# Kernel optimization log

Hardware: AMD Instinct MI355X
Metric: run time of the kernel (lower is better)

Reference implementation:

```python
import jax, jax.numpy as jnp
import numpy as np

B, W, N, L = 64, 256, 128, 64


def setup_inputs() -> dict:
    key = jax.random.key(0)
    k1, k2, k3 = jax.random.split(key, 3)
    x = jax.random.normal(k1, (B, W, L), dtype=jnp.float32)
    shapelets = jax.random.normal(k2, (N, L), dtype=jnp.float32)
    cls_w = jax.random.normal(k3, (1, N), dtype=jnp.float32) * 0.1
    cls_b = jnp.zeros((1,), dtype=jnp.float32)
    return {"x": x, "shapelets": shapelets, "cls_w": cls_w, "cls_b": cls_b}


def reference(x, shapelets, cls_w, cls_b):
    # diffs: [B, W, N, L] broadcast subtract
    diffs = x[:, :, None, :] - shapelets[None, None, :, :]
    # L2 norm over shapelet-length axis -> [B, W, N]
    discrim = jnp.sqrt(jnp.sum(diffs * diffs, axis=3))
    # min over windows -> [B, N]
    min_discrim = jnp.min(discrim, axis=1)
    # tiny classifier: Linear(N, 1) + sigmoid -> [B, 1]
    logits = min_discrim @ cls_w.T + cls_b
    return jax.nn.sigmoid(logits)
```

## Files before the change

kernel.cpp:

```cpp
#include <hip/hip_runtime.h>
#include <cfloat>
#include <cmath>

constexpr int B = 64;
constexpr int W = 256;
constexpr int N = 128;
constexpr int L = 64;
constexpr int NC = 16;
constexpr int WPB = W / NC;

__global__ __launch_bounds__(256) void shapelet_min_kernel(
    const float* __restrict__ x, const float* __restrict__ shp,
    float* __restrict__ part) {
  __shared__ float xs[WPB * L];
  __shared__ float xnorm_s[WPB];

  const int b = blockIdx.x >> 4;
  const int c = blockIdx.x & 15;
  const int tid = threadIdx.x;
  const int n = tid >> 1;
  const int half = tid & 1;

  {
    const float4* xg =
        (const float4*)(x + ((size_t)b * W + (size_t)c * WPB) * L);
    float4 v = xg[tid];
    ((float4*)xs)[tid] = v;
    float p = v.x * v.x + v.y * v.y + v.z * v.z + v.w * v.w;
    p += __shfl_xor(p, 8, 16);
    p += __shfl_xor(p, 4, 16);
    p += __shfl_xor(p, 2, 16);
    p += __shfl_xor(p, 1, 16);
    if ((tid & 15) == 0) xnorm_s[tid >> 4] = p;
  }

  const float4* sg = (const float4*)(shp + (size_t)n * L + half * 32);
  const float4 s0 = sg[0], s1 = sg[1], s2 = sg[2], s3 = sg[3];
  const float4 s4 = sg[4], s5 = sg[5], s6 = sg[6], s7 = sg[7];

  __syncthreads();

  float best = FLT_MAX;
  for (int w = 0; w < WPB; ++w) {
    const float4* xr = (const float4*)(xs + (size_t)w * L + half * 32);
    float a0 = 0.f, a1 = 0.f, a2 = 0.f, a3 = 0.f;
#define SHP_STEP(K, SV)              \
  {                                  \
    float4 xv = xr[K];               \
    a0 = fmaf(xv.x, (SV).x, a0);     \
    a1 = fmaf(xv.y, (SV).y, a1);     \
    a2 = fmaf(xv.z, (SV).z, a2);     \
    a3 = fmaf(xv.w, (SV).w, a3);     \
  }
    SHP_STEP(0, s0) SHP_STEP(1, s1) SHP_STEP(2, s2) SHP_STEP(3, s3)
    SHP_STEP(4, s4) SHP_STEP(5, s5) SHP_STEP(6, s6) SHP_STEP(7, s7)
#undef SHP_STEP
    float d = (a0 + a1) + (a2 + a3);
    d += __shfl_xor(d, 1, 64);
    best = fminf(best, fmaf(-2.f, d, xnorm_s[w]));
  }

  if (half == 0) {
    part[((size_t)b * NC + c) * N + n] = best;
  }
}

__global__ __launch_bounds__(128) void shapelet_head_kernel(
    const float* __restrict__ part, const float* __restrict__ shp,
    const float* __restrict__ cls_w, const float* __restrict__ cls_b,
    float* __restrict__ out) {
  const int b = blockIdx.x;
  const int n = threadIdx.x;

  float m = FLT_MAX;
#pragma unroll
  for (int c = 0; c < NC; ++c)
    m = fminf(m, part[((size_t)b * NC + c) * N + n]);

  float sn = 0.f;
  {
    const float4* sg = (const float4*)(shp + (size_t)n * L);
#pragma unroll
    for (int i = 0; i < L / 4; ++i) {
      float4 v = sg[i];
      sn = fmaf(v.x, v.x, sn);
      sn = fmaf(v.y, v.y, sn);
      sn = fmaf(v.z, v.z, sn);
      sn = fmaf(v.w, v.w, sn);
    }
  }

  float d2 = fmaxf(m + sn, 0.f);
  float v = sqrtf(d2) * cls_w[n];

#pragma unroll
  for (int off = 32; off > 0; off >>= 1) v += __shfl_down(v, off, 64);

  __shared__ float red[2];
  if ((n & 63) == 0) red[n >> 6] = v;
  __syncthreads();
  if (n == 0) {
    float z = red[0] + red[1] + cls_b[0];
    out[b] = 1.0f / (1.0f + expf(-z));
  }
}

extern "C" void kernel_launch(void* const* d_in, const int* in_sizes, int n_in,
                              void* d_out, int out_size, void* d_ws,
                              size_t ws_size, hipStream_t stream) {
  const float* x = (const float*)d_in[0];
  const float* shp = (const float*)d_in[1];
  const float* cls_w = (const float*)d_in[2];
  const float* cls_b = (const float*)d_in[3];
  float* out = (float*)d_out;
  float* part = (float*)d_ws;

  shapelet_min_kernel<<<B * NC, 256, 0, stream>>>(x, shp, part);
  shapelet_head_kernel<<<B, 128, 0, stream>>>(part, shp, cls_w, cls_b, out);
}
```

Measured before the change: 71.32 us.

## Register-block four shapelets per thread with 8-way split over length

```diff
diff --git a/kernel.cpp b/kernel.cpp
--- a/kernel.cpp
+++ b/kernel.cpp
@@ -18,8 +18,9 @@
   const int b = blockIdx.x >> 4;
   const int c = blockIdx.x & 15;
   const int tid = threadIdx.x;
-  const int n = tid >> 1;
-  const int half = tid & 1;
+  const int oct = tid & 7;
+  const int grp = tid >> 3;
+  const int n0 = grp * 4;
 
   {
     const float4* xg =
@@ -34,34 +35,58 @@
     if ((tid & 15) == 0) xnorm_s[tid >> 4] = p;
   }
 
-  const float4* sg = (const float4*)(shp + (size_t)n * L + half * 32);
-  const float4 s0 = sg[0], s1 = sg[1], s2 = sg[2], s3 = sg[3];
-  const float4 s4 = sg[4], s5 = sg[5], s6 = sg[6], s7 = sg[7];
+  const float4* g0 = (const float4*)(shp + (size_t)(n0 + 0) * L + oct * 8);
+  const float4* g1 = (const float4*)(shp + (size_t)(n0 + 1) * L + oct * 8);
+  const float4* g2 = (const float4*)(shp + (size_t)(n0 + 2) * L + oct * 8);
+  const float4* g3 = (const float4*)(shp + (size_t)(n0 + 3) * L + oct * 8);
+  const float4 s0a = g0[0], s0b = g0[1];
+  const float4 s1a = g1[0], s1b = g1[1];
+  const float4 s2a = g2[0], s2b = g2[1];
+  const float4 s3a = g3[0], s3b = g3[1];
 
   __syncthreads();
 
-  float best = FLT_MAX;
+  float best0 = FLT_MAX, best1 = FLT_MAX, best2 = FLT_MAX, best3 = FLT_MAX;
   for (int w = 0; w < WPB; ++w) {
-    const float4* xr = (const float4*)(xs + (size_t)w * L + half * 32);
-    float a0 = 0.f, a1 = 0.f, a2 = 0.f, a3 = 0.f;
-#define SHP_STEP(K, SV)              \
-  {                                  \
-    float4 xv = xr[K];               \
-    a0 = fmaf(xv.x, (SV).x, a0);     \
-    a1 = fmaf(xv.y, (SV).y, a1);     \
-    a2 = fmaf(xv.z, (SV).z, a2);     \
-    a3 = fmaf(xv.w, (SV).w, a3);     \
-  }
-    SHP_STEP(0, s0) SHP_STEP(1, s1) SHP_STEP(2, s2) SHP_STEP(3, s3)
-    SHP_STEP(4, s4) SHP_STEP(5, s5) SHP_STEP(6, s6) SHP_STEP(7, s7)
-#undef SHP_STEP
-    float d = (a0 + a1) + (a2 + a3);
-    d += __shfl_xor(d, 1, 64);
-    best = fminf(best, fmaf(-2.f, d, xnorm_s[w]));
+    const float4* xr = (const float4*)(xs + (size_t)w * L + oct * 8);
+    const float4 xa = xr[0];
+    const float4 xb = xr[1];
+
+    float d0 = xa.x * s0a.x + xa.y * s0a.y;
+    float d1 = xa.x * s1a.x + xa.y * s1a.y;
+    float d2 = xa.x * s2a.x + xa.y * s2a.y;
+    float d3 = xa.x * s3a.x + xa.y * s3a.y;
+    d0 = fmaf(xa.z, s0a.z, d0); d0 = fmaf(xa.w, s0a.w, d0);
+    d1 = fmaf(xa.z, s1a.z, d1); d1 = fmaf(xa.w, s1a.w, d1);
+    d2 = fmaf(xa.z, s2a.z, d2); d2 = fmaf(xa.w, s2a.w, d2);
+    d3 = fmaf(xa.z, s3a.z, d3); d3 = fmaf(xa.w, s3a.w, d3);
+    d0 = fmaf(xb.x, s0b.x, d0); d0 = fmaf(xb.y, s0b.y, d0);
+    d1 = fmaf(xb.x, s1b.x, d1); d1 = fmaf(xb.y, s1b.y, d1);
+    d2 = fmaf(xb.x, s2b.x, d2); d2 = fmaf(xb.y, s2b.y, d2);
+    d3 = fmaf(xb.x, s3b.x, d3); d3 = fmaf(xb.y, s3b.y, d3);
+    d0 = fmaf(xb.z, s0b.z, d0); d0 = fmaf(xb.w, s0b.w, d0);
+    d1 = fmaf(xb.z, s1b.z, d1); d1 = fmaf(xb.w, s1b.w, d1);
+    d2 = fmaf(xb.z, s2b.z, d2); d2 = fmaf(xb.w, s2b.w, d2);
+    d3 = fmaf(xb.z, s3b.z, d3); d3 = fmaf(xb.w, s3b.w, d3);
+
+    d0 += __shfl_xor(d0, 1, 64); d1 += __shfl_xor(d1, 1, 64);
+    d2 += __shfl_xor(d2, 1, 64); d3 += __shfl_xor(d3, 1, 64);
+    d0 += __shfl_xor(d0, 2, 64); d1 += __shfl_xor(d1, 2, 64);
+    d2 += __shfl_xor(d2, 2, 64); d3 += __shfl_xor(d3, 2, 64);
+    d0 += __shfl_xor(d0, 4, 64); d1 += __shfl_xor(d1, 4, 64);
+    d2 += __shfl_xor(d2, 4, 64); d3 += __shfl_xor(d3, 4, 64);
+
+    const float xn = xnorm_s[w];
+    best0 = fminf(best0, fmaf(-2.f, d0, xn));
+    best1 = fminf(best1, fmaf(-2.f, d1, xn));
+    best2 = fminf(best2, fmaf(-2.f, d2, xn));
+    best3 = fminf(best3, fmaf(-2.f, d3, xn));
   }
 
-  if (half == 0) {
-    part[((size_t)b * NC + c) * N + n] = best;
+  if (oct == 0) {
+    float4 o;
+    o.x = best0; o.y = best1; o.z = best2; o.w = best3;
+    *(float4*)(part + ((size_t)b * NC + c) * N + n0) = o;
   }
 }
 
```

After: 73.15 us. +2.6%, slower.
